# Performance work log

Measured on AMD Instinct MI355X. Metric: run time of the kernel, lower is better.

Reference implementation:

```python
import jax, jax.numpy as jnp
import numpy as np
from jax import lax


def _conv1x1(x, w, b=None):
    # x: [B,C,H,W], w: [O,C]
    y = jnp.einsum('bchw,oc->bohw', x, w)
    if b is not None:
        y = y + b[None, :, None, None]
    return y


def _lgce(x, pre_w, pre_b, w1, b1, w2, b2, sw, sb, post_w, post_b):
    # Local Group Context Enhancer on [B,64,H,W], 8 groups of 8 channels.
    b, c, h, wd = x.shape
    g = 8
    cg = c // g
    res = x
    x = _conv1x1(x, pre_w, pre_b)
    xg = x.reshape(b, g, cg, h, wd)
    # CBAM per group (vectorized over groups)
    pooled = xg.mean(axis=(3, 4))                                  # [b,g,cg]
    hid = jax.nn.relu(jnp.einsum('bgc,ghc->bgh', pooled, w1) + b1[None])
    cw = jax.nn.sigmoid(jnp.einsum('bgh,gch->bgc', hid, w2) + b2[None])
    xc = xg * cw[:, :, :, None, None]                              # channel gate
    sp = jax.nn.sigmoid(jnp.einsum('bgchw,goc->bgohw', xc, sw) + sb[None, :, :, None, None])
    cbam_out = xc * sp                                             # spatial gate
    resp = jax.nn.sigmoid(cbam_out)
    thr = resp.mean(axis=(2, 3, 4), keepdims=True)                 # per (batch, group)
    mask = jnp.where(resp > thr, jnp.ones_like(resp), resp)
    x = (xg * mask).reshape(b, c, h, wd)
    x = _conv1x1(x, post_w, post_b)
    return x + res


def setup_inputs() -> dict:
    key = jax.random.key(0)
    ks = jax.random.split(key, 20)
    f = lambda k, s: (jax.random.normal(k, s) * 0.02).astype(jnp.float32)
    return {
        'x': jax.random.normal(ks[0], (4, 128, 256, 256), dtype=jnp.float32),
        'input_proj_w': f(ks[1], (128, 128)),
        'lgce_pre_w': f(ks[2], (64, 64)), 'lgce_pre_b': f(ks[3], (64,)),
        'cbam_w1': f(ks[4], (8, 2, 8)), 'cbam_b1': f(ks[5], (8, 2)),
        'cbam_w2': f(ks[6], (8, 8, 2)), 'cbam_b2': f(ks[7], (8, 8)),
        'cbam_sw': f(ks[8], (8, 1, 8)), 'cbam_sb': f(ks[9], (8, 1)),
        'lgce_post_w': f(ks[10], (64, 64)), 'lgce_post_b': f(ks[11], (64,)),
        'qkv_w': f(ks[12], (192, 64)),
        'dw_w': f(ks[13], (192, 1, 3, 3)),
        'gate_w1': f(ks[14], (32, 64)), 'gate_b1': f(ks[15], (32,)),
        'gate_w2': f(ks[16], (1, 32)), 'gate_b2': f(ks[17], (1,)),
        'temperature': jnp.ones((8, 1, 1), jnp.float32),
        'scales': jnp.full((4,), 0.2, jnp.float32),
        'proj_out_w': f(ks[18], (128, 128)),
    }


def reference(x, input_proj_w, lgce_pre_w, lgce_pre_b, cbam_w1, cbam_b1,
              cbam_w2, cbam_b2, cbam_sw, cbam_sb, lgce_post_w, lgce_post_b,
              qkv_w, dw_w, gate_w1, gate_b1, gate_w2, gate_b2,
              temperature, scales, proj_out_w):
    b, c, h, wd = x.shape
    heads = 8
    proj = _conv1x1(x, input_proj_w)
    lb, gb = jnp.split(proj, 2, axis=1)                            # local / global
    lb = _lgce(lb, lgce_pre_w, lgce_pre_b, cbam_w1, cbam_b1, cbam_w2, cbam_b2,
               cbam_sw, cbam_sb, lgce_post_w, lgce_post_b)
    qkv = _conv1x1(gb, qkv_w)
    qkv = lax.conv_general_dilated(qkv, dw_w, (1, 1), 'SAME',
                                   feature_group_count=192,
                                   dimension_numbers=('NCHW', 'OIHW', 'NCHW'))
    q, k, v = jnp.split(qkv, 3, axis=1)
    hw = h * wd
    cph = (c // 2) // heads                                        # channels per head
    to_heads = lambda t: t.reshape(b, heads, cph, hw)
    q, k, v = to_heads(q), to_heads(k), to_heads(v)
    q = q / jnp.maximum(jnp.linalg.norm(q, axis=-1, keepdims=True), 1e-12)
    k = k / jnp.maximum(jnp.linalg.norm(k, axis=-1, keepdims=True), 1e-12)
    attn = jnp.einsum('bhcn,bhdn->bhcd', q, k) * temperature[None]  # [b,h,cph,cph]
    # dynamic top-k from global gate (single scalar over whole batch, as original)
    gate = jax.nn.sigmoid(_conv1x1(jax.nn.relu(_conv1x1(gb, gate_w1, gate_b1)),
                                   gate_w2, gate_b2))
    kdyn = jnp.clip(jnp.floor(cph * gate.mean()), 1.0, float(cph))
    # rank-based top-k mask (jit-safe equivalent of topk+scatter)
    ranks = jnp.argsort(jnp.argsort(-attn, axis=-1), axis=-1)
    attn = jnp.where(ranks < kdyn, attn, -jnp.inf)
    attn = jax.nn.softmax(attn, axis=-1)
    out = jnp.einsum('bhcd,bhdn->bhcn', attn, v) * scales.sum()
    out = out.reshape(b, c // 2, h, wd)
    fused = jnp.concatenate([out, lb], axis=1)
    return _conv1x1(fused, proj_out_w)
```

## Files before the change

kernel.cpp:

```cpp
#include <hip/hip_runtime.h>
#include <math.h>

#define HWN 65536

__device__ __forceinline__ float sgm(float x){ return 1.0f/(1.0f+expf(-x)); }

__device__ __forceinline__ void fma4(float acc[4], const float4 w,
                                     const float4 x0, const float4 x1,
                                     const float4 x2, const float4 x3){
    acc[0] += w.x*x0.x + w.y*x1.x + w.z*x2.x + w.w*x3.x;
    acc[1] += w.x*x0.y + w.y*x1.y + w.z*x2.y + w.w*x3.y;
    acc[2] += w.x*x0.z + w.y*x1.z + w.z*x2.z + w.w*x3.z;
    acc[3] += w.x*x0.w + w.y*x1.w + w.z*x2.w + w.w*x3.w;
}

__global__ __launch_bounds__(256,2) void k1_proj(
    const float* __restrict__ x,   const float* __restrict__ Wp,
    const float* __restrict__ Wpre,const float* __restrict__ bpre,
    const float* __restrict__ Wqkv,
    const float* __restrict__ Wg1, const float* __restrict__ bg1,
    const float* __restrict__ wg2, const float* __restrict__ bg2,
    float* __restrict__ lb, float* __restrict__ pre, float* __restrict__ qkv,
    float* __restrict__ pooled_part, float* __restrict__ gate_part)
{
    __shared__ float st[128*128];
    float4* st4 = (float4*)st;
    float*  ht  = st;

    const int t    = threadIdx.x;
    const int blk  = blockIdx.x;
    const int b    = blk >> 9;
    const int p0   = (blk & 511) << 7;
    const int pg   = t & 15;
    const int og   = t >> 4;
    const int slot = blk & 63;

    const float4* x4 = (const float4*)x;

    #pragma unroll
    for (int i = 0; i < 16; ++i) {
        int idx = t + 256*i;
        int c = idx >> 5, q = idx & 31;
        st4[c*32 + q] = x4[(size_t)(b*128 + c)*16384 + (p0>>2) + q];
    }
    __syncthreads();

    {
        const int o0 = og*8;
        float acc[8][8];
        #pragma unroll
        for (int j=0;j<8;++j)
            #pragma unroll
            for (int k=0;k<8;++k) acc[j][k]=0.f;
        const float4* W4 = (const float4*)Wp;
        for (int c = 0; c < 128; c += 4) {
            float4 xa0 = st4[(c+0)*32 + pg],      xb0 = st4[(c+0)*32 + 16 + pg];
            float4 xa1 = st4[(c+1)*32 + pg],      xb1 = st4[(c+1)*32 + 16 + pg];
            float4 xa2 = st4[(c+2)*32 + pg],      xb2 = st4[(c+2)*32 + 16 + pg];
            float4 xa3 = st4[(c+3)*32 + pg],      xb3 = st4[(c+3)*32 + 16 + pg];
            #pragma unroll
            for (int j = 0; j < 8; ++j) {
                float4 w = W4[(o0+j)*32 + (c>>2)];
                fma4(&acc[j][0], w, xa0,xa1,xa2,xa3);
                fma4(&acc[j][4], w, xb0,xb1,xb2,xb3);
            }
        }
        __syncthreads();

        #pragma unroll
        for (int j = 0; j < 8; ++j) {
            st4[(o0+j)*32 + pg]      = make_float4(acc[j][0],acc[j][1],acc[j][2],acc[j][3]);
            st4[(o0+j)*32 + 16 + pg] = make_float4(acc[j][4],acc[j][5],acc[j][6],acc[j][7]);
        }
        if (og < 8) {
            float4* lb4 = (float4*)lb;
            #pragma unroll
            for (int j = 0; j < 8; ++j) {
                lb4[(size_t)(b*64 + o0+j)*16384 + (p0>>2) + pg] =
                    make_float4(acc[j][0],acc[j][1],acc[j][2],acc[j][3]);
                lb4[(size_t)(b*64 + o0+j)*16384 + (p0>>2) + 16 + pg] =
                    make_float4(acc[j][4],acc[j][5],acc[j][6],acc[j][7]);
            }
        }
    }
    __syncthreads();

    {
        const int o0 = og*4;
        float acc[4][8];
        #pragma unroll
        for (int j=0;j<4;++j)
            #pragma unroll
            for (int k=0;k<8;++k) acc[j][k]=0.f;
        const float4* W4 = (const float4*)Wpre;
        for (int c = 0; c < 64; c += 4) {
            float4 xa0 = st4[(c+0)*32 + pg],      xb0 = st4[(c+0)*32 + 16 + pg];
            float4 xa1 = st4[(c+1)*32 + pg],      xb1 = st4[(c+1)*32 + 16 + pg];
            float4 xa2 = st4[(c+2)*32 + pg],      xb2 = st4[(c+2)*32 + 16 + pg];
            float4 xa3 = st4[(c+3)*32 + pg],      xb3 = st4[(c+3)*32 + 16 + pg];
            #pragma unroll
            for (int j = 0; j < 4; ++j) {
                float4 w = W4[(o0+j)*16 + (c>>2)];
                fma4(&acc[j][0], w, xa0,xa1,xa2,xa3);
                fma4(&acc[j][4], w, xb0,xb1,xb2,xb3);
            }
        }
        float4* pre4 = (float4*)pre;
        #pragma unroll
        for (int j = 0; j < 4; ++j) {
            float bs = bpre[o0+j];
            float4 v0 = make_float4(acc[j][0]+bs, acc[j][1]+bs, acc[j][2]+bs, acc[j][3]+bs);
            float4 v1 = make_float4(acc[j][4]+bs, acc[j][5]+bs, acc[j][6]+bs, acc[j][7]+bs);
            pre4[(size_t)(b*64 + o0+j)*16384 + (p0>>2) + pg]      = v0;
            pre4[(size_t)(b*64 + o0+j)*16384 + (p0>>2) + 16 + pg] = v1;
            float s = v0.x+v0.y+v0.z+v0.w + v1.x+v1.y+v1.z+v1.w;
            s += __shfl_xor(s,1); s += __shfl_xor(s,2);
            s += __shfl_xor(s,4); s += __shfl_xor(s,8);
            if (pg == 0) atomicAdd(&pooled_part[slot*256 + b*64 + o0 + j], s);
        }
    }

    #pragma unroll
    for (int chk = 0; chk < 2; ++chk) {
        const int o0 = og*12 + chk*6;
        float acc[6][8];
        #pragma unroll
        for (int j=0;j<6;++j)
            #pragma unroll
            for (int k=0;k<8;++k) acc[j][k]=0.f;
        const float4* W4 = (const float4*)Wqkv;
        for (int c = 0; c < 64; c += 4) {
            float4 xa0 = st4[(64+c+0)*32 + pg],   xb0 = st4[(64+c+0)*32 + 16 + pg];
            float4 xa1 = st4[(64+c+1)*32 + pg],   xb1 = st4[(64+c+1)*32 + 16 + pg];
            float4 xa2 = st4[(64+c+2)*32 + pg],   xb2 = st4[(64+c+2)*32 + 16 + pg];
            float4 xa3 = st4[(64+c+3)*32 + pg],   xb3 = st4[(64+c+3)*32 + 16 + pg];
            #pragma unroll
            for (int j = 0; j < 6; ++j) {
                float4 w = W4[(o0+j)*16 + (c>>2)];
                fma4(&acc[j][0], w, xa0,xa1,xa2,xa3);
                fma4(&acc[j][4], w, xb0,xb1,xb2,xb3);
            }
        }
        float4* qkv4 = (float4*)qkv;
        #pragma unroll
        for (int j = 0; j < 6; ++j) {
            qkv4[(size_t)(b*192 + o0+j)*16384 + (p0>>2) + pg] =
                make_float4(acc[j][0],acc[j][1],acc[j][2],acc[j][3]);
            qkv4[(size_t)(b*192 + o0+j)*16384 + (p0>>2) + 16 + pg] =
                make_float4(acc[j][4],acc[j][5],acc[j][6],acc[j][7]);
        }
    }

    {
        const int o0 = og*2;
        float acc[2][8];
        #pragma unroll
        for (int j=0;j<2;++j)
            #pragma unroll
            for (int k=0;k<8;++k) acc[j][k]=0.f;
        const float4* W4 = (const float4*)Wg1;
        for (int c = 0; c < 64; c += 4) {
            float4 xa0 = st4[(64+c+0)*32 + pg],   xb0 = st4[(64+c+0)*32 + 16 + pg];
            float4 xa1 = st4[(64+c+1)*32 + pg],   xb1 = st4[(64+c+1)*32 + 16 + pg];
            float4 xa2 = st4[(64+c+2)*32 + pg],   xb2 = st4[(64+c+2)*32 + 16 + pg];
            float4 xa3 = st4[(64+c+3)*32 + pg],   xb3 = st4[(64+c+3)*32 + 16 + pg];
            #pragma unroll
            for (int j = 0; j < 2; ++j) {
                float4 w = W4[(o0+j)*16 + (c>>2)];
                fma4(&acc[j][0], w, xa0,xa1,xa2,xa3);
                fma4(&acc[j][4], w, xb0,xb1,xb2,xb3);
            }
        }
        __syncthreads();
        #pragma unroll
        for (int j = 0; j < 2; ++j) {
            float bs = bg1[o0+j];
            #pragma unroll
            for (int k = 0; k < 4; ++k) {
                ht[(o0+j)*128 + pg*4 + k]      = fmaxf(acc[j][k]+bs,   0.0f);
                ht[(o0+j)*128 + 64 + pg*4 + k] = fmaxf(acc[j][4+k]+bs, 0.0f);
            }
        }
    }
    __syncthreads();

    if (t < 128) {
        float g = bg2[0];
        #pragma unroll
        for (int c = 0; c < 32; ++c) g += wg2[c]*ht[c*128 + t];
        g = sgm(g);
        g += __shfl_xor(g,1);  g += __shfl_xor(g,2);  g += __shfl_xor(g,4);
        g += __shfl_xor(g,8);  g += __shfl_xor(g,16); g += __shfl_xor(g,32);
        if ((t & 63) == 0) atomicAdd(&gate_part[slot], g);
    }
}

__global__ void k2_small(const float* __restrict__ pooled_part,
                         const float* __restrict__ gate_part,
                         const float* __restrict__ w1, const float* __restrict__ b1,
                         const float* __restrict__ w2, const float* __restrict__ b2,
                         float* __restrict__ cw, float* __restrict__ kdyn)
{
    __shared__ float pl[256];
    const int t = threadIdx.x;
    float s = 0.f;
    for (int sl = 0; sl < 64; ++sl) s += pooled_part[sl*256 + t];
    pl[t] = s * (1.0f/65536.0f);
    __syncthreads();
    const int b = t >> 6, g = (t >> 3) & 7, c = t & 7;
    float h0 = b1[g*2+0], h1 = b1[g*2+1];
    #pragma unroll
    for (int cc = 0; cc < 8; ++cc) {
        float p = pl[b*64 + g*8 + cc];
        h0 += p*w1[g*16 + 0*8 + cc];
        h1 += p*w1[g*16 + 1*8 + cc];
    }
    h0 = fmaxf(h0, 0.f); h1 = fmaxf(h1, 0.f);
    cw[t] = sgm(h0*w2[g*16 + c*2 + 0] + h1*w2[g*16 + c*2 + 1] + b2[g*8+c]);
    if (t == 0) {
        float gs = 0.f;
        for (int sl = 0; sl < 64; ++sl) gs += gate_part[sl];
        float kd = floorf(8.0f * (gs * (1.0f/262144.0f)));
        *kdyn = fminf(fmaxf(kd, 1.0f), 8.0f);
    }
}

__global__ __launch_bounds__(256) void k3_thr(
    const float* __restrict__ pre, const float* __restrict__ cw,
    const float* __restrict__ sw,  const float* __restrict__ sb,
    float* __restrict__ thr_sum)
{
    __shared__ float part[4][8];
    const int t = threadIdx.x;
    const int b = blockIdx.x >> 8;
    const int p = ((blockIdx.x & 255) << 8) + t;
    float rs[8];
    #pragma unroll
    for (int g = 0; g < 8; ++g) {
        float xc[8];
        float spa = sb[g];
        #pragma unroll
        for (int c = 0; c < 8; ++c) {
            float xv = pre[(size_t)(b*64 + g*8 + c)*HWN + p];
            xc[c] = xv * cw[b*64 + g*8 + c];
            spa += xc[c]*sw[g*8 + c];
        }
        float sp = sgm(spa);
        float s = 0.f;
        #pragma unroll
        for (int c = 0; c < 8; ++c) s += sgm(xc[c]*sp);
        rs[g] = s;
    }
    const int lane = t & 63, wv = t >> 6;
    #pragma unroll
    for (int g = 0; g < 8; ++g) {
        float val = rs[g];
        val += __shfl_xor(val,1);  val += __shfl_xor(val,2);  val += __shfl_xor(val,4);
        val += __shfl_xor(val,8);  val += __shfl_xor(val,16); val += __shfl_xor(val,32);
        if (lane == 0) part[wv][g] = val;
    }
    __syncthreads();
    if (t < 8)
        atomicAdd(&thr_sum[b*8 + t], part[0][t]+part[1][t]+part[2][t]+part[3][t]);
}

#define K4_ROWSTRIDE 264
#define K4_BUF (10*K4_ROWSTRIDE)

__global__ __launch_bounds__(256,3) void k4_dw(
    const float* __restrict__ qkv, const float* __restrict__ dww,
    float* __restrict__ v, float* __restrict__ Sg, float* __restrict__ sumsq)
{
    __shared__ float sh[2*K4_BUF];

    const int t    = threadIdx.x;
    const int b    = blockIdx.x >> 8;
    const int h    = (blockIdx.x >> 5) & 7;
    const int band = blockIdx.x & 31;
    const int r0   = band * 8;
    const int lr   = t >> 5;
    const int c0   = (t & 31) * 4;
    const int lane = t & 63;

    if (t < 40) {
        int bufi = t / 20, r = (t % 20) >> 1, side = t & 1;
        sh[bufi*K4_BUF + r*K4_ROWSTRIDE + (side ? 260 : 3)] = 0.0f;
    }

    float4 reg[3];

    auto issue_loads = [&](int ch) {
        const float4* base = (const float4*)(qkv + (size_t)(b*192 + ch)*HWN);
        #pragma unroll
        for (int j = 0; j < 3; ++j) {
            int i = t + 256*j;
            float4 val = make_float4(0.f,0.f,0.f,0.f);
            if (i < 640) {
                int row = i >> 6, col4 = i & 63;
                int gy = r0 - 1 + row;
                if (gy >= 0 && gy < 256) val = base[gy*64 + col4];
            }
            reg[j] = val;
        }
    };

    auto write_lds = [&](float* buf) {
        #pragma unroll
        for (int j = 0; j < 3; ++j) {
            int i = t + 256*j;
            if (i < 640) {
                int row = i >> 6, col4 = i & 63;
                *(float4*)&buf[row*K4_ROWSTRIDE + 4 + col4*4] = reg[j];
            }
        }
    };

    auto conv8 = [&](const float* buf, const float* __restrict__ w9, float out[8]) {
        #pragma unroll
        for (int g = 0; g < 2; ++g) {
            const int cc = c0 + g*128;
            float a0=0.f, a1=0.f, a2=0.f, a3=0.f;
            #pragma unroll
            for (int rr = 0; rr < 3; ++rr) {
                const float* row = &buf[(lr+rr)*K4_ROWSTRIDE + 4 + cc];
                float4 m = *(const float4*)row;
                float l = row[-1], r = row[4];
                float w0 = w9[rr*3+0], w1 = w9[rr*3+1], w2 = w9[rr*3+2];
                a0 = fmaf(w0,l,   fmaf(w1,m.x, fmaf(w2,m.y, a0)));
                a1 = fmaf(w0,m.x, fmaf(w1,m.y, fmaf(w2,m.z, a1)));
                a2 = fmaf(w0,m.y, fmaf(w1,m.z, fmaf(w2,m.w, a2)));
                a3 = fmaf(w0,m.z, fmaf(w1,m.w, fmaf(w2,r,   a3)));
            }
            out[g*4+0]=a0; out[g*4+1]=a1; out[g*4+2]=a2; out[g*4+3]=a3;
        }
    };

    auto wsum = [&](float val) {
        val += __shfl_xor(val,1);  val += __shfl_xor(val,2);  val += __shfl_xor(val,4);
        val += __shfl_xor(val,8);  val += __shfl_xor(val,16); val += __shfl_xor(val,32);
        return val;
    };

    float dq[8][8];

    float* sq_q = &sumsq[b*128 + h*8];
    float* sq_k = &sumsq[b*128 + 64 + h*8];
    float* Sgb  = &Sg[(size_t)(b*8+h)*64];

    issue_loads(h*8 + 0);

    #pragma unroll
    for (int ch = 0; ch < 8; ++ch) {
        float* buf = sh + (ch & 1)*K4_BUF;
        write_lds(buf);
        issue_loads(ch < 7 ? (h*8 + ch + 1) : (64 + h*8));
        __syncthreads();
        conv8(buf, dww + (h*8 + ch)*9, dq[ch]);
        float ss = 0.f;
        #pragma unroll
        for (int p = 0; p < 8; ++p) ss = fmaf(dq[ch][p], dq[ch][p], ss);
        ss = wsum(ss);
        if (lane == 0) atomicAdd(&sq_q[ch], ss);
    }

    #pragma unroll
    for (int ch = 0; ch < 8; ++ch) {
        float* buf = sh + (ch & 1)*K4_BUF;
        write_lds(buf);
        issue_loads(ch < 7 ? (64 + h*8 + ch + 1) : (128 + h*8));
        __syncthreads();
        float dk[8];
        conv8(buf, dww + (64 + h*8 + ch)*9, dk);
        float ss = 0.f;
        #pragma unroll
        for (int p = 0; p < 8; ++p) ss = fmaf(dk[p], dk[p], ss);
        ss = wsum(ss);
        if (lane == 0) atomicAdd(&sq_k[ch], ss);
        #pragma unroll
        for (int c = 0; c < 8; ++c) {
            float acc = 0.f;
            #pragma unroll
            for (int p = 0; p < 8; ++p) acc = fmaf(dq[c][p], dk[p], acc);
            acc = wsum(acc);
            if (lane == 0) atomicAdd(&Sgb[c*8 + ch], acc);
        }
    }

    #pragma unroll
    for (int ch = 0; ch < 8; ++ch) {
        float* buf = sh + (ch & 1)*K4_BUF;
        write_lds(buf);
        if (ch < 7) issue_loads(128 + h*8 + ch + 1);
        __syncthreads();
        float dv[8];
        conv8(buf, dww + (128 + h*8 + ch)*9, dv);
        float* vb = v + (size_t)(b*64 + h*8 + ch)*HWN + (r0 + lr)*256;
        *(float4*)&vb[c0]       = make_float4(dv[0],dv[1],dv[2],dv[3]);
        *(float4*)&vb[c0 + 128] = make_float4(dv[4],dv[5],dv[6],dv[7]);
    }
}

__global__ void k6_attn(const float* __restrict__ Sg, const float* __restrict__ sumsq,
                        const float* __restrict__ temp, const float* __restrict__ kdynp,
                        const float* __restrict__ thr_sum, const float* __restrict__ scales,
                        float* __restrict__ A, float* __restrict__ thr)
{
    const int t = threadIdx.x;
    if (t < 32) thr[t] = thr_sum[t] * (1.0f/(8.0f*65536.0f));
    const int b = t >> 6, h = (t >> 3) & 7, c = t & 7;
    const float kd = *kdynp;
    const float ssum = scales[0]+scales[1]+scales[2]+scales[3];
    const float nq = fmaxf(sqrtf(sumsq[b*128 + h*8 + c]), 1e-12f);
    const float tv = temp[h];
    const float* Srow = Sg + (size_t)(b*8+h)*64 + c*8;
    float a[8];
    #pragma unroll
    for (int d = 0; d < 8; ++d) {
        float nk = fmaxf(sqrtf(sumsq[b*128 + 64 + h*8 + d]), 1e-12f);
        a[d] = Srow[d] / (nq*nk) * tv;
    }
    bool keep[8];
    #pragma unroll
    for (int d = 0; d < 8; ++d) {
        int r = 0;
        #pragma unroll
        for (int e = 0; e < 8; ++e)
            r += (a[e] > a[d]) || (a[e] == a[d] && e < d);
        keep[d] = ((float)r < kd);
    }
    float m = -INFINITY;
    #pragma unroll
    for (int d = 0; d < 8; ++d) if (keep[d]) m = fmaxf(m, a[d]);
    float ex[8]; float sum = 0.f;
    #pragma unroll
    for (int d = 0; d < 8; ++d) { ex[d] = keep[d] ? expf(a[d]-m) : 0.f; sum += ex[d]; }
    const float inv = ssum / sum;
    #pragma unroll
    for (int d = 0; d < 8; ++d)
        A[(size_t)(b*8+h)*64 + c*8 + d] = ex[d]*inv;
}

__global__ __launch_bounds__(256,2) void k7_final(
    const float* __restrict__ pre, const float* __restrict__ lb, const float* __restrict__ v,
    const float* __restrict__ cw,  const float* __restrict__ thr,
    const float* __restrict__ sw,  const float* __restrict__ sb,
    const float* __restrict__ A,
    const float* __restrict__ Wpost, const float* __restrict__ bpost,
    const float* __restrict__ Wout,  float* __restrict__ out)
{
    __shared__ float pr[64*64];
    __shared__ float vt[64*64];
    __shared__ float ft[128*64];
    float4* pr4 = (float4*)pr;
    float4* vt4 = (float4*)vt;
    float4* ft4 = (float4*)ft;

    const int t   = threadIdx.x;
    const int blk = blockIdx.x;
    const int b   = blk >> 10;
    const int p0  = (blk & 1023) << 6;
    const int pg  = t & 15;
    const int og  = t >> 4;

    const float4* pre4g = (const float4*)pre;
    const float4* v4g   = (const float4*)v;
    #pragma unroll
    for (int i = 0; i < 4; ++i) {
        int idx = t + 256*i;
        int c = idx >> 4, q = idx & 15;
        size_t gi = (size_t)(b*64 + c)*16384 + (p0>>2) + q;
        pr4[c*16+q] = pre4g[gi];
        vt4[c*16+q] = v4g[gi];
    }
    __syncthreads();

    #pragma unroll
    for (int s = 0; s < 2; ++s) {
        int task = t + 256*s;
        int g = task >> 6, px = task & 63;
        float xc[8], xv[8];
        float spa = sb[g];
        #pragma unroll
        for (int c = 0; c < 8; ++c) {
            xv[c] = pr[(g*8+c)*64 + px];
            xc[c] = xv[c]*cw[b*64 + g*8 + c];
            spa += xc[c]*sw[g*8 + c];
        }
        float sp = sgm(spa);
        float th = thr[b*8 + g];
        #pragma unroll
        for (int c = 0; c < 8; ++c) {
            float resp = sgm(xc[c]*sp);
            float mask = resp > th ? 1.0f : resp;
            pr[(g*8+c)*64 + px] = xv[c]*mask;
        }
    }
    __syncthreads();

    {
        const int o0 = og*4;
        float acc[4][4];
        #pragma unroll
        for (int j=0;j<4;++j){acc[j][0]=0.f;acc[j][1]=0.f;acc[j][2]=0.f;acc[j][3]=0.f;}
        const float4* W4 = (const float4*)Wpost;
        for (int c = 0; c < 64; c += 4) {
            float4 x0 = pr4[(c+0)*16+pg];
            float4 x1 = pr4[(c+1)*16+pg];
            float4 x2 = pr4[(c+2)*16+pg];
            float4 x3 = pr4[(c+3)*16+pg];
            #pragma unroll
            for (int j=0;j<4;++j)
                fma4(acc[j], W4[(o0+j)*16 + (c>>2)], x0,x1,x2,x3);
        }
        const float4* lb4 = (const float4*)lb;
        #pragma unroll
        for (int j=0;j<4;++j){
            float bs = bpost[o0+j];
            float4 lv = lb4[(size_t)(b*64 + o0+j)*16384 + (p0>>2) + pg];
            ft4[(64+o0+j)*16 + pg] = make_float4(acc[j][0]+bs+lv.x, acc[j][1]+bs+lv.y,
                                                 acc[j][2]+bs+lv.z, acc[j][3]+bs+lv.w);
        }
    }

    {
        const int ch0 = og*4;
        #pragma unroll
        for (int j = 0; j < 4; ++j) {
            int ch = ch0 + j;
            int hh = ch >> 3, c = ch & 7;
            const float* Ar = A + (size_t)(b*8+hh)*64 + c*8;
            float4 acc = make_float4(0.f,0.f,0.f,0.f);
            #pragma unroll
            for (int d = 0; d < 8; ++d) {
                float av = Ar[d];
                float4 vv = vt4[(hh*8+d)*16 + pg];
                acc.x += av*vv.x; acc.y += av*vv.y; acc.z += av*vv.z; acc.w += av*vv.w;
            }
            ft4[ch*16 + pg] = acc;
        }
    }
    __syncthreads();

    {
        const int o0 = og*8;
        float acc[8][4];
        #pragma unroll
        for (int j=0;j<8;++j){acc[j][0]=0.f;acc[j][1]=0.f;acc[j][2]=0.f;acc[j][3]=0.f;}
        const float4* W4 = (const float4*)Wout;
        for (int c = 0; c < 128; c += 4) {
            float4 x0 = ft4[(c+0)*16+pg];
            float4 x1 = ft4[(c+1)*16+pg];
            float4 x2 = ft4[(c+2)*16+pg];
            float4 x3 = ft4[(c+3)*16+pg];
            #pragma unroll
            for (int j=0;j<8;++j)
                fma4(acc[j], W4[(o0+j)*32 + (c>>2)], x0,x1,x2,x3);
        }
        float4* out4 = (float4*)out;
        #pragma unroll
        for (int j=0;j<8;++j)
            out4[(size_t)(b*128 + o0+j)*16384 + (p0>>2) + pg] =
                make_float4(acc[j][0],acc[j][1],acc[j][2],acc[j][3]);
    }
}

extern "C" void kernel_launch(void* const* d_in, const int* in_sizes, int n_in,
                              void* d_out, int out_size, void* d_ws, size_t ws_size,
                              hipStream_t stream)
{
    const float* x     = (const float*)d_in[0];
    const float* Wp    = (const float*)d_in[1];
    const float* Wpre  = (const float*)d_in[2];
    const float* bpre  = (const float*)d_in[3];
    const float* w1    = (const float*)d_in[4];
    const float* b1    = (const float*)d_in[5];
    const float* w2    = (const float*)d_in[6];
    const float* b2    = (const float*)d_in[7];
    const float* sw    = (const float*)d_in[8];
    const float* sb    = (const float*)d_in[9];
    const float* Wpost = (const float*)d_in[10];
    const float* bpost = (const float*)d_in[11];
    const float* Wqkv  = (const float*)d_in[12];
    const float* dww   = (const float*)d_in[13];
    const float* Wg1   = (const float*)d_in[14];
    const float* bg1   = (const float*)d_in[15];
    const float* wg2   = (const float*)d_in[16];
    const float* bg2   = (const float*)d_in[17];
    const float* temp  = (const float*)d_in[18];
    const float* scales= (const float*)d_in[19];
    const float* Wout  = (const float*)d_in[20];
    float* out = (float*)d_out;

    float* ws = (float*)d_ws;
    float* pooled_part = ws;
    float* gate_part   = ws + 16384;
    float* thr_sum     = ws + 16448;
    float* sumsq       = ws + 16480;
    float* Sg          = ws + 16992;
    float* cw          = ws + 19040;
    float* kdyn        = ws + 19296;
    float* thr         = ws + 19328;
    float* A           = ws + 19360;

    float* lb  = ws + 32768;
    float* pre = lb  + 16777216;
    float* qkv = pre + 16777216;
    float* v   = qkv + 50331648;

    hipMemsetAsync(ws, 0, (size_t)19040*sizeof(float), stream);

    k1_proj <<<2048, 256, 0, stream>>>(x, Wp, Wpre, bpre, Wqkv, Wg1, bg1, wg2, bg2,
                                       lb, pre, qkv, pooled_part, gate_part);
    k2_small<<<1,    256, 0, stream>>>(pooled_part, gate_part, w1, b1, w2, b2, cw, kdyn);
    k3_thr  <<<1024, 256, 0, stream>>>(pre, cw, sw, sb, thr_sum);
    k4_dw   <<<1024, 256, 0, stream>>>(qkv, dww, v, Sg, sumsq);
    k6_attn <<<1,    256, 0, stream>>>(Sg, sumsq, temp, kdyn, thr_sum, scales, A, thr);
    k7_final<<<4096, 256, 0, stream>>>(pre, lb, v, cw, thr, sw, sb, A,
                                       Wpost, bpost, Wout, out);
}
```

Measured before the change: 850.1 us.

## Double k7_final pixel tile to 128 and reuse shared buffers for fused features

```diff
diff --git a/kernel.cpp b/kernel.cpp
--- a/kernel.cpp
+++ b/kernel.cpp
@@ -448,41 +448,39 @@
     const float* __restrict__ Wpost, const float* __restrict__ bpost,
     const float* __restrict__ Wout,  float* __restrict__ out)
 {
-    __shared__ float pr[64*64];
-    __shared__ float vt[64*64];
-    __shared__ float ft[128*64];
+    __shared__ float pr[64*128];
+    __shared__ float vt[64*128];
     float4* pr4 = (float4*)pr;
     float4* vt4 = (float4*)vt;
-    float4* ft4 = (float4*)ft;
 
     const int t   = threadIdx.x;
     const int blk = blockIdx.x;
-    const int b   = blk >> 10;
-    const int p0  = (blk & 1023) << 6;
+    const int b   = blk >> 9;
+    const int p0  = (blk & 511) << 7;
     const int pg  = t & 15;
     const int og  = t >> 4;
 
     const float4* pre4g = (const float4*)pre;
     const float4* v4g   = (const float4*)v;
     #pragma unroll
-    for (int i = 0; i < 4; ++i) {
+    for (int i = 0; i < 8; ++i) {
         int idx = t + 256*i;
-        int c = idx >> 4, q = idx & 15;
+        int c = idx >> 5, q = idx & 31;
         size_t gi = (size_t)(b*64 + c)*16384 + (p0>>2) + q;
-        pr4[c*16+q] = pre4g[gi];
-        vt4[c*16+q] = v4g[gi];
-    }
-    __syncthreads();
-
-    #pragma unroll
-    for (int s = 0; s < 2; ++s) {
+        pr4[c*32+q] = pre4g[gi];
+        vt4[c*32+q] = v4g[gi];
+    }
+    __syncthreads();
+
+    #pragma unroll
+    for (int s = 0; s < 4; ++s) {
         int task = t + 256*s;
-        int g = task >> 6, px = task & 63;
+        int g = task >> 7, px = task & 127;
         float xc[8], xv[8];
         float spa = sb[g];
         #pragma unroll
         for (int c = 0; c < 8; ++c) {
-            xv[c] = pr[(g*8+c)*64 + px];
+            xv[c] = pr[(g*8+c)*128 + px];
             xc[c] = xv[c]*cw[b*64 + g*8 + c];
             spa += xc[c]*sw[g*8 + c];
         }
@@ -492,36 +490,46 @@
         for (int c = 0; c < 8; ++c) {
             float resp = sgm(xc[c]*sp);
             float mask = resp > th ? 1.0f : resp;
-            pr[(g*8+c)*64 + px] = xv[c]*mask;
-        }
-    }
-    __syncthreads();
-
+            pr[(g*8+c)*128 + px] = xv[c]*mask;
+        }
+    }
+    __syncthreads();
+
+    float postv[4][8];
     {
         const int o0 = og*4;
-        float acc[4][4];
-        #pragma unroll
-        for (int j=0;j<4;++j){acc[j][0]=0.f;acc[j][1]=0.f;acc[j][2]=0.f;acc[j][3]=0.f;}
+        float acc[4][8];
+        #pragma unroll
+        for (int j=0;j<4;++j)
+            #pragma unroll
+            for (int k=0;k<8;++k) acc[j][k]=0.f;
         const float4* W4 = (const float4*)Wpost;
         for (int c = 0; c < 64; c += 4) {
-            float4 x0 = pr4[(c+0)*16+pg];
-            float4 x1 = pr4[(c+1)*16+pg];
-            float4 x2 = pr4[(c+2)*16+pg];
-            float4 x3 = pr4[(c+3)*16+pg];
-            #pragma unroll
-            for (int j=0;j<4;++j)
-                fma4(acc[j], W4[(o0+j)*16 + (c>>2)], x0,x1,x2,x3);
+            float4 xa0 = pr4[(c+0)*32 + pg],      xb0 = pr4[(c+0)*32 + 16 + pg];
+            float4 xa1 = pr4[(c+1)*32 + pg],      xb1 = pr4[(c+1)*32 + 16 + pg];
+            float4 xa2 = pr4[(c+2)*32 + pg],      xb2 = pr4[(c+2)*32 + 16 + pg];
+            float4 xa3 = pr4[(c+3)*32 + pg],      xb3 = pr4[(c+3)*32 + 16 + pg];
+            #pragma unroll
+            for (int j = 0; j < 4; ++j) {
+                float4 w = W4[(o0+j)*16 + (c>>2)];
+                fma4(&acc[j][0], w, xa0,xa1,xa2,xa3);
+                fma4(&acc[j][4], w, xb0,xb1,xb2,xb3);
+            }
         }
         const float4* lb4 = (const float4*)lb;
         #pragma unroll
-        for (int j=0;j<4;++j){
+        for (int j = 0; j < 4; ++j) {
             float bs = bpost[o0+j];
-            float4 lv = lb4[(size_t)(b*64 + o0+j)*16384 + (p0>>2) + pg];
-            ft4[(64+o0+j)*16 + pg] = make_float4(acc[j][0]+bs+lv.x, acc[j][1]+bs+lv.y,
-                                                 acc[j][2]+bs+lv.z, acc[j][3]+bs+lv.w);
-        }
-    }
-
+            float4 l0 = lb4[(size_t)(b*64 + o0+j)*16384 + (p0>>2) + pg];
+            float4 l1 = lb4[(size_t)(b*64 + o0+j)*16384 + (p0>>2) + 16 + pg];
+            postv[j][0]=acc[j][0]+bs+l0.x; postv[j][1]=acc[j][1]+bs+l0.y;
+            postv[j][2]=acc[j][2]+bs+l0.z; postv[j][3]=acc[j][3]+bs+l0.w;
+            postv[j][4]=acc[j][4]+bs+l1.x; postv[j][5]=acc[j][5]+bs+l1.y;
+            postv[j][6]=acc[j][6]+bs+l1.z; postv[j][7]=acc[j][7]+bs+l1.w;
+        }
+    }
+
+    float attv[4][8];
     {
         const int ch0 = og*4;
         #pragma unroll
@@ -529,38 +537,73 @@
             int ch = ch0 + j;
             int hh = ch >> 3, c = ch & 7;
             const float* Ar = A + (size_t)(b*8+hh)*64 + c*8;
-            float4 acc = make_float4(0.f,0.f,0.f,0.f);
+            float a0=0.f,a1=0.f,a2=0.f,a3=0.f,a4=0.f,a5=0.f,a6=0.f,a7=0.f;
             #pragma unroll
             for (int d = 0; d < 8; ++d) {
                 float av = Ar[d];
-                float4 vv = vt4[(hh*8+d)*16 + pg];
-                acc.x += av*vv.x; acc.y += av*vv.y; acc.z += av*vv.z; acc.w += av*vv.w;
-            }
-            ft4[ch*16 + pg] = acc;
+                float4 v0 = vt4[(hh*8+d)*32 + pg];
+                float4 v1 = vt4[(hh*8+d)*32 + 16 + pg];
+                a0 += av*v0.x; a1 += av*v0.y; a2 += av*v0.z; a3 += av*v0.w;
+                a4 += av*v1.x; a5 += av*v1.y; a6 += av*v1.z; a7 += av*v1.w;
+            }
+            attv[j][0]=a0; attv[j][1]=a1; attv[j][2]=a2; attv[j][3]=a3;
+            attv[j][4]=a4; attv[j][5]=a5; attv[j][6]=a6; attv[j][7]=a7;
+        }
+    }
+    __syncthreads();
+
+    {
+        const int o0 = og*4;
+        #pragma unroll
+        for (int j = 0; j < 4; ++j) {
+            vt4[(o0+j)*32 + pg]      = make_float4(attv[j][0],attv[j][1],attv[j][2],attv[j][3]);
+            vt4[(o0+j)*32 + 16 + pg] = make_float4(attv[j][4],attv[j][5],attv[j][6],attv[j][7]);
+            pr4[(o0+j)*32 + pg]      = make_float4(postv[j][0],postv[j][1],postv[j][2],postv[j][3]);
+            pr4[(o0+j)*32 + 16 + pg] = make_float4(postv[j][4],postv[j][5],postv[j][6],postv[j][7]);
         }
     }
     __syncthreads();
 
     {
         const int o0 = og*8;
-        float acc[8][4];
-        #pragma unroll
-        for (int j=0;j<8;++j){acc[j][0]=0.f;acc[j][1]=0.f;acc[j][2]=0.f;acc[j][3]=0.f;}
+        float acc[8][8];
+        #pragma unroll
+        for (int j=0;j<8;++j)
+            #pragma unroll
+            for (int k=0;k<8;++k) acc[j][k]=0.f;
         const float4* W4 = (const float4*)Wout;
-        for (int c = 0; c < 128; c += 4) {
-            float4 x0 = ft4[(c+0)*16+pg];
-            float4 x1 = ft4[(c+1)*16+pg];
-            float4 x2 = ft4[(c+2)*16+pg];
-            float4 x3 = ft4[(c+3)*16+pg];
-            #pragma unroll
-            for (int j=0;j<8;++j)
-                fma4(acc[j], W4[(o0+j)*32 + (c>>2)], x0,x1,x2,x3);
+        for (int c = 0; c < 64; c += 4) {
+            float4 xa0 = vt4[(c+0)*32 + pg],      xb0 = vt4[(c+0)*32 + 16 + pg];
+            float4 xa1 = vt4[(c+1)*32 + pg],      xb1 = vt4[(c+1)*32 + 16 + pg];
+            float4 xa2 = vt4[(c+2)*32 + pg],      xb2 = vt4[(c+2)*32 + 16 + pg];
+            float4 xa3 = vt4[(c+3)*32 + pg],      xb3 = vt4[(c+3)*32 + 16 + pg];
+            #pragma unroll
+            for (int j = 0; j < 8; ++j) {
+                float4 w = W4[(o0+j)*32 + (c>>2)];
+                fma4(&acc[j][0], w, xa0,xa1,xa2,xa3);
+                fma4(&acc[j][4], w, xb0,xb1,xb2,xb3);
+            }
+        }
+        for (int c = 0; c < 64; c += 4) {
+            float4 xa0 = pr4[(c+0)*32 + pg],      xb0 = pr4[(c+0)*32 + 16 + pg];
+            float4 xa1 = pr4[(c+1)*32 + pg],      xb1 = pr4[(c+1)*32 + 16 + pg];
+            float4 xa2 = pr4[(c+2)*32 + pg],      xb2 = pr4[(c+2)*32 + 16 + pg];
+            float4 xa3 = pr4[(c+3)*32 + pg],      xb3 = pr4[(c+3)*32 + 16 + pg];
+            #pragma unroll
+            for (int j = 0; j < 8; ++j) {
+                float4 w = W4[(o0+j)*32 + 16 + (c>>2)];
+                fma4(&acc[j][0], w, xa0,xa1,xa2,xa3);
+                fma4(&acc[j][4], w, xb0,xb1,xb2,xb3);
+            }
         }
         float4* out4 = (float4*)out;
         #pragma unroll
-        for (int j=0;j<8;++j)
+        for (int j = 0; j < 8; ++j) {
             out4[(size_t)(b*128 + o0+j)*16384 + (p0>>2) + pg] =
                 make_float4(acc[j][0],acc[j][1],acc[j][2],acc[j][3]);
+            out4[(size_t)(b*128 + o0+j)*16384 + (p0>>2) + 16 + pg] =
+                make_float4(acc[j][4],acc[j][5],acc[j][6],acc[j][7]);
+        }
     }
 }
 
@@ -615,6 +658,6 @@
     k3_thr  <<<1024, 256, 0, stream>>>(pre, cw, sw, sb, thr_sum);
     k4_dw   <<<1024, 256, 0, stream>>>(qkv, dww, v, Sg, sumsq);
     k6_attn <<<1,    256, 0, stream>>>(Sg, sumsq, temp, kdyn, thr_sum, scales, A, thr);
-    k7_final<<<4096, 256, 0, stream>>>(pre, lb, v, cw, thr, sw, sb, A,
+    k7_final<<<2048, 256, 0, stream>>>(pre, lb, v, cw, thr, sw, sb, A,
                                        Wpost, bpost, Wout, out);
 }
```

After: 807.3 us. -5.0%, faster.
